# Optimization experiments

Measured on AMD Instinct MI355X. Metric: run time of the kernel, lower is better.

## Reference

```python
import jax, jax.numpy as jnp
import numpy as np

D_MODEL = 1024
N_HEADS = 16
D_K = D_MODEL // N_HEADS


def setup_inputs() -> dict:
    key = jax.random.key(0)
    ks = jax.random.split(key, 12)
    B, S, D = 4, 2048, D_MODEL
    scale = 1.0 / np.sqrt(D)
    inp = {
        'query': jax.random.normal(ks[0], (B, S, D), jnp.float32),
        'key': jax.random.normal(ks[1], (B, S, D), jnp.float32),
        'value': jax.random.normal(ks[2], (B, S, D), jnp.float32),
        'Wq': jax.random.normal(ks[3], (D, D), jnp.float32) * scale,
        'bq': jax.random.normal(ks[4], (D,), jnp.float32) * 0.02,
        'Wk': jax.random.normal(ks[5], (D, D), jnp.float32) * scale,
        'bk': jax.random.normal(ks[6], (D,), jnp.float32) * 0.02,
        'Wv': jax.random.normal(ks[7], (D, D), jnp.float32) * scale,
        'bv': jax.random.normal(ks[8], (D,), jnp.float32) * 0.02,
        'Wo': jax.random.normal(ks[9], (D, D), jnp.float32) * scale,
        'bo': jax.random.normal(ks[10], (D,), jnp.float32) * 0.02,
    }
    return inp


def reference(query, key, value, Wq, bq, Wk, bk, Wv, bv, Wo, bo):
    B, S, D = query.shape
    # torch nn.Linear: y = x @ W^T + b
    def proj(x, W, b):
        y = jnp.einsum('bsd,ed->bse', x, W) + b
        # [B,S,D] -> [B,H,S,d_k]
        return y.reshape(B, S, N_HEADS, D_K).transpose(0, 2, 1, 3)

    q = proj(query, Wq, bq)
    k = proj(key, Wk, bk)
    v = proj(value, Wv, bv)

    scores = jnp.einsum('bhqd,bhkd->bhqk', q, k) / jnp.sqrt(jnp.float32(D_K))
    attn = jax.nn.softmax(scores, axis=-1)  # dropout = identity (eval mode)
    out = jnp.einsum('bhqk,bhkd->bhqd', attn, v)
    out = out.transpose(0, 2, 1, 3).reshape(B, S, D)
    return jnp.einsum('bsd,ed->bse', out, Wo) + bo
```

## Files before the change

### kernel.cpp

```cpp
#include <hip/hip_runtime.h>
#include <hip/hip_bf16.h>
#include <cstdint>
#include <cstddef>


#define BATCH   4
#define SEQ     2048
#define D_MODEL 1024
#define NHEADS  16
#define DK      64

typedef __attribute__((ext_vector_type(8))) __bf16 bf16x8_t;
typedef __attribute__((ext_vector_type(4))) float  f32x4;

__device__ inline unsigned int pack2(float lo, float hi) {
  __hip_bfloat162 h = __float22bfloat162_rn(make_float2(lo, hi));
  union { __hip_bfloat162 h; unsigned int u; } c; c.h = h; return c.u;
}
__device__ inline unsigned short f2bf(float f) { return (unsigned short)pack2(f, f); }

#if __has_builtin(__builtin_amdgcn_exp2f)
__device__ inline float fexp2(float x) { return __builtin_amdgcn_exp2f(x); }
#else
__device__ inline float fexp2(float x) { return __expf(x * 0.6931471805599453f); }
#endif

__device__ inline void cvt8(const float* __restrict__ s, unsigned short* __restrict__ d) {
  const float4 a = *(const float4*)s;
  const float4 b = *(const float4*)(s + 4);
  uint4 r;
  r.x = pack2(a.x, a.y); r.y = pack2(a.z, a.w);
  r.z = pack2(b.x, b.y); r.w = pack2(b.z, b.w);
  *(uint4*)d = r;
}

typedef __attribute__((address_space(3))) unsigned int lds_u32_t;
typedef const __attribute__((address_space(1))) unsigned int glb_u32_t;
__device__ inline void gld16(const unsigned short* g, unsigned short* l) {
  __builtin_amdgcn_global_load_lds((glb_u32_t*)(uintptr_t)g,
                                   (lds_u32_t*)(unsigned int)(uintptr_t)l, 16, 0, 0);
}

__global__ __launch_bounds__(256) void cvt3_kernel(
    const float* __restrict__ a, const float* __restrict__ b, const float* __restrict__ c,
    unsigned short* __restrict__ oa, unsigned short* __restrict__ ob, unsigned short* __restrict__ oc)
{
  const float* s = (blockIdx.y == 0) ? a : (blockIdx.y == 1) ? b : c;
  unsigned short* d = (blockIdx.y == 0) ? oa : (blockIdx.y == 1) ? ob : oc;
  const size_t i = ((size_t)blockIdx.x * 256 + threadIdx.x) * 8;
  cvt8(s + i, d + i);
}
__global__ __launch_bounds__(256) void cvt4_kernel(
    const float* __restrict__ a, const float* __restrict__ b,
    const float* __restrict__ c, const float* __restrict__ dd,
    unsigned short* __restrict__ oa, unsigned short* __restrict__ ob,
    unsigned short* __restrict__ oc, unsigned short* __restrict__ od)
{
  const float* s = (blockIdx.y == 0) ? a : (blockIdx.y == 1) ? b : (blockIdx.y == 2) ? c : dd;
  unsigned short* d = (blockIdx.y == 0) ? oa : (blockIdx.y == 1) ? ob : (blockIdx.y == 2) ? oc : od;
  const size_t i = ((size_t)blockIdx.x * 256 + threadIdx.x) * 8;
  cvt8(s + i, d + i);
}

__device__ inline void gemm_core(const unsigned short* __restrict__ A,
                                 const unsigned short* __restrict__ W,
                                 unsigned short* a_lds, unsigned short* b_lds,
                                 int m0, int n0, f32x4 (&acc)[4][4])
{
  const int tid  = threadIdx.x;
  const int lane = tid & 63;
  const int wv   = tid >> 6;
  const int l15  = lane & 15;
  const int quad = lane >> 4;
  const int wm = (wv & 1) * 64;
  const int wn = (wv >> 1) * 64;

  const int srow = tid >> 2;
  const int sch  = (tid & 3) ^ (srow & 3);
  const unsigned short* Ap0 = A + (size_t)(m0 + srow) * D_MODEL + sch * 8;
  const unsigned short* Ap1 = Ap0 + (size_t)64 * D_MODEL;
  const unsigned short* Wp0 = W + (size_t)(n0 + srow) * D_MODEL + sch * 8;
  const unsigned short* Wp1 = Wp0 + (size_t)64 * D_MODEL;
  unsigned short* al0 = a_lds + wv * 512;
  unsigned short* al1 = a_lds + 2048 + wv * 512;
  unsigned short* bl0 = b_lds + wv * 512;
  unsigned short* bl1 = b_lds + 2048 + wv * 512;

  const int pq = (quad ^ (l15 & 3)) * 8;

  for (int k0 = 0; k0 < D_MODEL; k0 += 32) {
    __syncthreads();
    gld16(Ap0 + k0, al0);
    gld16(Ap1 + k0, al1);
    gld16(Wp0 + k0, bl0);
    gld16(Wp1 + k0, bl1);
    __syncthreads();

    bf16x8_t af[4], bfr[4];
#pragma unroll
    for (int i = 0; i < 4; ++i)
      af[i] = *(const bf16x8_t*)&a_lds[(wm + i * 16 + l15) * 32 + pq];
#pragma unroll
    for (int j = 0; j < 4; ++j)
      bfr[j] = *(const bf16x8_t*)&b_lds[(wn + j * 16 + l15) * 32 + pq];

#pragma unroll
    for (int i = 0; i < 4; ++i)
#pragma unroll
      for (int j = 0; j < 4; ++j)
        acc[i][j] = __builtin_amdgcn_mfma_f32_16x16x32_bf16(af[i], bfr[j], acc[i][j], 0, 0, 0);
  }
}

__global__ __launch_bounds__(256) void qkv_kernel(
    const unsigned short* __restrict__ qb, const unsigned short* __restrict__ kb,
    const unsigned short* __restrict__ vb,
    const unsigned short* __restrict__ wq, const unsigned short* __restrict__ wk,
    const unsigned short* __restrict__ wvp,
    const float* __restrict__ bq, const float* __restrict__ bk, const float* __restrict__ bv,
    unsigned short* __restrict__ Qws, unsigned short* __restrict__ Kws,
    unsigned short* __restrict__ Vws)
{
  __shared__ unsigned short a_lds[128 * 32];
  __shared__ unsigned short b_lds[128 * 32];

  const int z = blockIdx.z;
  const unsigned short* A = (z == 0) ? qb : (z == 1) ? kb : vb;
  const unsigned short* W = (z == 0) ? wq : (z == 1) ? wk : wvp;
  const float* bias       = (z == 0) ? bq : (z == 1) ? bk : bv;
  unsigned short* C       = (z == 0) ? Qws : (z == 1) ? Kws : Vws;
  const int m0 = blockIdx.x * 128;
  const int n0 = blockIdx.y * 128;

  f32x4 acc[4][4];
#pragma unroll
  for (int i = 0; i < 4; ++i)
#pragma unroll
    for (int j = 0; j < 4; ++j)
      acc[i][j] = (f32x4){0.f, 0.f, 0.f, 0.f};

  gemm_core(A, W, a_lds, b_lds, m0, n0, acc);

  const int tid  = threadIdx.x;
  const int lane = tid & 63;
  const int wv   = tid >> 6;
  const int l15  = lane & 15;
  const int quad = lane >> 4;
  const int wm = (wv & 1) * 64;
  const int wn = (wv >> 1) * 64;
  if (z == 2) {
    for (int j = 0; j < 4; ++j) {
      const int n = n0 + wn + j * 16 + l15;
      const int hh = n >> 6, dd = n & 63;
      const float bvl = bias[n];
      for (int i = 0; i < 4; ++i) {
        const int mbase = m0 + wm + i * 16 + quad * 4;
        const int bb = mbase >> 11, ss = mbase & 2047;
        uint2 w2 = make_uint2(pack2(acc[i][j][0] + bvl, acc[i][j][1] + bvl),
                              pack2(acc[i][j][2] + bvl, acc[i][j][3] + bvl));
        *(uint2*)(C + (((size_t)bb * NHEADS + hh) * DK + dd) * SEQ + ss) = w2;
      }
    }
  } else {
    const float oscale = (z == 0) ? 0.18033688011112042f : 1.0f;
    for (int j = 0; j < 4; ++j) {
      const int n = n0 + wn + j * 16 + l15;
      const int hh = n >> 6, dd = n & 63;
      const float bvl = bias[n];
      for (int i = 0; i < 4; ++i) {
        const int mbase = m0 + wm + i * 16 + quad * 4;
        const int bb = mbase >> 11, ss = mbase & 2047;
        unsigned short* dst = C + (((size_t)bb * NHEADS + hh) * SEQ + ss) * DK + dd;
        for (int r = 0; r < 4; ++r)
          dst[(size_t)r * DK] = f2bf((acc[i][j][r] + bvl) * oscale);
      }
    }
  }
}

__global__ __launch_bounds__(256) void outproj_kernel(
    const unsigned short* __restrict__ A, const unsigned short* __restrict__ W,
    const float* __restrict__ bias, float* __restrict__ C)
{
  __shared__ unsigned short a_lds[128 * 32];
  __shared__ unsigned short b_lds[128 * 32];
  const int m0 = blockIdx.x * 128;
  const int n0 = blockIdx.y * 128;

  f32x4 acc[4][4];
#pragma unroll
  for (int i = 0; i < 4; ++i)
#pragma unroll
    for (int j = 0; j < 4; ++j)
      acc[i][j] = (f32x4){0.f, 0.f, 0.f, 0.f};

  gemm_core(A, W, a_lds, b_lds, m0, n0, acc);

  const int tid  = threadIdx.x;
  const int lane = tid & 63;
  const int wv   = tid >> 6;
  const int l15  = lane & 15;
  const int quad = lane >> 4;
  const int wm = (wv & 1) * 64;
  const int wn = (wv >> 1) * 64;
  for (int j = 0; j < 4; ++j) {
    const int n = n0 + wn + j * 16 + l15;
    const float bvl = bias[n];
    for (int i = 0; i < 4; ++i) {
      const int mbase = m0 + wm + i * 16 + quad * 4;
      for (int r = 0; r < 4; ++r)
        C[(size_t)(mbase + r) * D_MODEL + n] = acc[i][j][r] + bvl;
    }
  }
}

__global__ __launch_bounds__(256) void attn_kernel(
    const unsigned short* __restrict__ Q,
    const unsigned short* __restrict__ K,
    const unsigned short* __restrict__ Vt,
    unsigned short* __restrict__ Oattn)
{
  __shared__ unsigned short k_sw[64 * 64];
  __shared__ unsigned short vt_sw[64 * 64];
  __shared__ unsigned short pt_sw[4 * 16 * 64];

  const int tid  = threadIdx.x;
  const int lane = tid & 63;
  const int wv   = tid >> 6;
  const int l15  = lane & 15;
  const int quad = lane >> 4;
  const int bh   = blockIdx.x;
  const int q0   = blockIdx.y * 64;
  const size_t hoff = (size_t)bh * SEQ * DK;
  const unsigned short* Qh  = Q  + hoff;
  const unsigned short* Kh  = K  + hoff;
  const unsigned short* Vth = Vt + hoff;

  bf16x8_t qf0, qf1;
  {
    const unsigned short* qr = Qh + (size_t)(q0 + wv * 16 + l15) * DK;
    qf0 = *(const bf16x8_t*)(qr + quad * 8);
    qf1 = *(const bf16x8_t*)(qr + 32 + quad * 8);
  }

  f32x4 o[4];
#pragma unroll
  for (int t = 0; t < 4; ++t) o[t] = (f32x4){0.f, 0.f, 0.f, 0.f};
  float mval = -1e30f, lval = 0.f;

  const int sr = lane >> 3;
  const int pc = lane & 7;
  const int r0 = wv * 16 + sr;
  const int r1 = r0 + 8;
  const int sem0 = pc ^ (r0 & 7) ^ (r0 >> 3);
  const int sem1 = pc ^ (r1 & 7) ^ (r1 >> 3);
  const unsigned short* Ks0 = Kh  + (size_t)r0 * DK  + sem0 * 8;
  const unsigned short* Ks1 = Kh  + (size_t)r1 * DK  + sem1 * 8;
  const unsigned short* Vs0 = Vth + (size_t)r0 * SEQ + sem0 * 8;
  const unsigned short* Vs1 = Vth + (size_t)r1 * SEQ + sem1 * 8;
  unsigned short* kd0 = k_sw  + wv * 1024;
  unsigned short* kd1 = k_sw  + wv * 1024 + 512;
  unsigned short* vd0 = vt_sw + wv * 1024;
  unsigned short* vd1 = vt_sw + wv * 1024 + 512;

  const int swz_l15 = (l15 & 7) ^ (l15 >> 3);
  unsigned short* pt_base = pt_sw + wv * 1024;

  for (int kb = 0; kb < SEQ / 64; ++kb) {
    const int key0 = kb * 64;
    __syncthreads();
    gld16(Ks0 + (size_t)key0 * DK, kd0);
    gld16(Ks1 + (size_t)key0 * DK, kd1);
    gld16(Vs0 + key0, vd0);
    gld16(Vs1 + key0, vd1);
    __syncthreads();

    f32x4 s[4];
#pragma unroll
    for (int t = 0; t < 4; ++t) {
      const int row = t * 16 + l15;
      const int sw  = (row & 7) ^ (row >> 3);
      bf16x8_t kf0 = *(const bf16x8_t*)&k_sw[row * 64 + ((quad ^ sw) << 3)];
      bf16x8_t kf1 = *(const bf16x8_t*)&k_sw[row * 64 + (((quad | 4) ^ sw) << 3)];
      f32x4 z = (f32x4){0.f, 0.f, 0.f, 0.f};
      z = __builtin_amdgcn_mfma_f32_16x16x32_bf16(kf0, qf0, z, 0, 0, 0);
      z = __builtin_amdgcn_mfma_f32_16x16x32_bf16(kf1, qf1, z, 0, 0, 0);
      s[t] = z;
    }

    float mx = s[0][0];
#pragma unroll
    for (int t = 0; t < 4; ++t)
#pragma unroll
      for (int r = 0; r < 4; ++r) mx = fmaxf(mx, s[t][r]);
    mx = fmaxf(mx, __shfl_xor(mx, 16));
    mx = fmaxf(mx, __shfl_xor(mx, 32));
    const float mnew  = fmaxf(mval, mx);
    const float alpha = fexp2(mval - mnew);
    mval = mnew;
    float rs = 0.f;
    float p[4][4];
#pragma unroll
    for (int t = 0; t < 4; ++t)
#pragma unroll
      for (int r = 0; r < 4; ++r) { p[t][r] = fexp2(s[t][r] - mnew); rs += p[t][r]; }
    rs += __shfl_xor(rs, 16);
    rs += __shfl_xor(rs, 32);
    lval = lval * alpha + rs;
#pragma unroll
    for (int t = 0; t < 4; ++t) o[t] *= alpha;

#pragma unroll
    for (int t = 0; t < 4; ++t) {
      const int chunk = 2 * t + (quad >> 1);
      unsigned short* dst = pt_base + l15 * 64 + ((chunk ^ swz_l15) << 3) + (quad & 1) * 4;
      *(uint2*)dst = make_uint2(pack2(p[t][0], p[t][1]), pack2(p[t][2], p[t][3]));
    }
    asm volatile("s_waitcnt lgkmcnt(0)" ::: "memory");

    bf16x8_t pf0 = *(const bf16x8_t*)(pt_base + l15 * 64 + ((quad ^ swz_l15) << 3));
    bf16x8_t pf1 = *(const bf16x8_t*)(pt_base + l15 * 64 + (((quad | 4) ^ swz_l15) << 3));

#pragma unroll
    for (int nt = 0; nt < 4; ++nt) {
      const int row = nt * 16 + l15;
      const int sw  = (row & 7) ^ (row >> 3);
      bf16x8_t vf0 = *(const bf16x8_t*)&vt_sw[row * 64 + ((quad ^ sw) << 3)];
      bf16x8_t vf1 = *(const bf16x8_t*)&vt_sw[row * 64 + (((quad | 4) ^ sw) << 3)];
      o[nt] = __builtin_amdgcn_mfma_f32_16x16x32_bf16(vf0, pf0, o[nt], 0, 0, 0);
      o[nt] = __builtin_amdgcn_mfma_f32_16x16x32_bf16(vf1, pf1, o[nt], 0, 0, 0);
    }
  }

  const int bb = bh >> 4, hh = bh & 15;
  const float inv = 1.0f / lval;
  unsigned short* orow = Oattn + (size_t)(bb * SEQ + q0 + wv * 16 + l15) * D_MODEL + hh * DK + quad * 4;
#pragma unroll
  for (int nt = 0; nt < 4; ++nt) {
    f32x4 v = o[nt];
    *(uint2*)(orow + nt * 16) = make_uint2(pack2(v[0] * inv, v[1] * inv),
                                           pack2(v[2] * inv, v[3] * inv));
  }
}

extern "C" void kernel_launch(void* const* d_in, const int* in_sizes, int n_in,
                              void* d_out, int out_size, void* d_ws, size_t ws_size,
                              hipStream_t stream) {
  const float* query = (const float*)d_in[0];
  const float* key   = (const float*)d_in[1];
  const float* value = (const float*)d_in[2];
  const float* Wq    = (const float*)d_in[3];
  const float* bq    = (const float*)d_in[4];
  const float* Wk    = (const float*)d_in[5];
  const float* bk    = (const float*)d_in[6];
  const float* Wv    = (const float*)d_in[7];
  const float* bv    = (const float*)d_in[8];
  const float* Wo    = (const float*)d_in[9];
  const float* bo    = (const float*)d_in[10];

  const size_t E  = (size_t)BATCH * SEQ * D_MODEL;
  const size_t WE = (size_t)D_MODEL * D_MODEL;
  unsigned short* ws  = (unsigned short*)d_ws;
  unsigned short* Qws = ws;
  unsigned short* Kws = ws + E;
  unsigned short* Vws = ws + 2 * E;
  unsigned short* qb  = ws + 3 * E;
  unsigned short* kb  = ws + 4 * E;
  unsigned short* vb  = ws + 5 * E;
  unsigned short* wqb = ws + 6 * E;
  unsigned short* wkb = wqb + WE;
  unsigned short* wvb = wqb + 2 * WE;
  unsigned short* wob = wqb + 3 * WE;
  unsigned short* Aws = qb;

  cvt3_kernel<<<dim3(E / 2048, 3), 256, 0, stream>>>(query, key, value, qb, kb, vb);
  cvt4_kernel<<<dim3(WE / 2048, 4), 256, 0, stream>>>(Wq, Wk, Wv, Wo, wqb, wkb, wvb, wob);

  qkv_kernel<<<dim3(BATCH * SEQ / 128, D_MODEL / 128, 3), 256, 0, stream>>>(
      qb, kb, vb, wqb, wkb, wvb, bq, bk, bv, Qws, Kws, Vws);
  attn_kernel<<<dim3(BATCH * NHEADS, SEQ / 64), 256, 0, stream>>>(Qws, Kws, Vws, Aws);
  outproj_kernel<<<dim3(BATCH * SEQ / 128, D_MODEL / 128), 256, 0, stream>>>(
      Aws, wob, bo, (float*)d_out);
}
```

Before: 410.2 us.

## Double-buffer K/V tiles, lazily rescale softmax, and raise MFMA wave priority

The attention kernel now keeps two LDS buffers for K and V^T. It issues the global-to-LDS loads for the next key block before computing on the current one, which drops from two barriers per iteration to one. The online-softmax rescale of the output accumulator and running sum now runs only when some lane's block max exceeds the running max by more than 8 (log2 domain). Otherwise the stale max is kept and the exp/multiply work per block is skipped. s_setprio brackets the MFMA sections to favour matrix issue. The cost is double the K/V LDS footprint, which may lower occupancy, and unnormalised P values up to 2^8 before bf16 packing.

```diff
diff --git a/kernel.cpp b/kernel.cpp
--- a/kernel.cpp
+++ b/kernel.cpp
@@ -220,8 +220,8 @@
     const unsigned short* __restrict__ Vt,
     unsigned short* __restrict__ Oattn)
 {
-  __shared__ unsigned short k_sw[64 * 64];
-  __shared__ unsigned short vt_sw[64 * 64];
+  __shared__ unsigned short k_sw[2 * 64 * 64];
+  __shared__ unsigned short vt_sw[2 * 64 * 64];
   __shared__ unsigned short pt_sw[4 * 16 * 64];
 
   const int tid  = threadIdx.x;
@@ -254,39 +254,47 @@
   const int r1 = r0 + 8;
   const int sem0 = pc ^ (r0 & 7) ^ (r0 >> 3);
   const int sem1 = pc ^ (r1 & 7) ^ (r1 >> 3);
-  const unsigned short* Ks0 = Kh  + (size_t)r0 * DK  + sem0 * 8;
-  const unsigned short* Ks1 = Kh  + (size_t)r1 * DK  + sem1 * 8;
-  const unsigned short* Vs0 = Vth + (size_t)r0 * SEQ + sem0 * 8;
-  const unsigned short* Vs1 = Vth + (size_t)r1 * SEQ + sem1 * 8;
-  unsigned short* kd0 = k_sw  + wv * 1024;
-  unsigned short* kd1 = k_sw  + wv * 1024 + 512;
-  unsigned short* vd0 = vt_sw + wv * 1024;
-  unsigned short* vd1 = vt_sw + wv * 1024 + 512;
+  const unsigned short* KsA = Kh  + (size_t)r0 * DK  + sem0 * 8;
+  const unsigned short* KsB = Kh  + (size_t)r1 * DK  + sem1 * 8;
+  const unsigned short* VsA = Vth + (size_t)r0 * SEQ + sem0 * 8;
+  const unsigned short* VsB = Vth + (size_t)r1 * SEQ + sem1 * 8;
+  unsigned short* kd = k_sw  + wv * 1024;
+  unsigned short* vd = vt_sw + wv * 1024;
+
+#define STAGE(buf, key0) do {                                        \
+    gld16(KsA + (size_t)(key0) * DK, kd + (buf) * 4096);             \
+    gld16(KsB + (size_t)(key0) * DK, kd + (buf) * 4096 + 512);       \
+    gld16(VsA + (key0),              vd + (buf) * 4096);             \
+    gld16(VsB + (key0),              vd + (buf) * 4096 + 512);       \
+  } while (0)
 
   const int swz_l15 = (l15 & 7) ^ (l15 >> 3);
   unsigned short* pt_base = pt_sw + wv * 1024;
 
+  STAGE(0, 0);
+  __syncthreads();
+
+  int cur = 0;
   for (int kb = 0; kb < SEQ / 64; ++kb) {
-    const int key0 = kb * 64;
-    __syncthreads();
-    gld16(Ks0 + (size_t)key0 * DK, kd0);
-    gld16(Ks1 + (size_t)key0 * DK, kd1);
-    gld16(Vs0 + key0, vd0);
-    gld16(Vs1 + key0, vd1);
-    __syncthreads();
+    if (kb + 1 < SEQ / 64) STAGE(cur ^ 1, (kb + 1) * 64);
+
+    const unsigned short* kcur = k_sw  + cur * 4096;
+    const unsigned short* vcur = vt_sw + cur * 4096;
 
     f32x4 s[4];
+    __builtin_amdgcn_s_setprio(1);
 #pragma unroll
     for (int t = 0; t < 4; ++t) {
       const int row = t * 16 + l15;
       const int sw  = (row & 7) ^ (row >> 3);
-      bf16x8_t kf0 = *(const bf16x8_t*)&k_sw[row * 64 + ((quad ^ sw) << 3)];
-      bf16x8_t kf1 = *(const bf16x8_t*)&k_sw[row * 64 + (((quad | 4) ^ sw) << 3)];
+      bf16x8_t kf0 = *(const bf16x8_t*)&kcur[row * 64 + ((quad ^ sw) << 3)];
+      bf16x8_t kf1 = *(const bf16x8_t*)&kcur[row * 64 + (((quad | 4) ^ sw) << 3)];
       f32x4 z = (f32x4){0.f, 0.f, 0.f, 0.f};
       z = __builtin_amdgcn_mfma_f32_16x16x32_bf16(kf0, qf0, z, 0, 0, 0);
       z = __builtin_amdgcn_mfma_f32_16x16x32_bf16(kf1, qf1, z, 0, 0, 0);
       s[t] = z;
     }
+    __builtin_amdgcn_s_setprio(0);
 
     float mx = s[0][0];
 #pragma unroll
@@ -295,20 +303,23 @@
       for (int r = 0; r < 4; ++r) mx = fmaxf(mx, s[t][r]);
     mx = fmaxf(mx, __shfl_xor(mx, 16));
     mx = fmaxf(mx, __shfl_xor(mx, 32));
-    const float mnew  = fmaxf(mval, mx);
-    const float alpha = fexp2(mval - mnew);
-    mval = mnew;
+    if (__any(mx > mval + 8.0f)) {
+      const float mnew  = fmaxf(mval, mx);
+      const float alpha = fexp2(mval - mnew);
+      mval = mnew;
+      lval *= alpha;
+#pragma unroll
+      for (int t = 0; t < 4; ++t) o[t] *= alpha;
+    }
     float rs = 0.f;
     float p[4][4];
 #pragma unroll
     for (int t = 0; t < 4; ++t)
 #pragma unroll
-      for (int r = 0; r < 4; ++r) { p[t][r] = fexp2(s[t][r] - mnew); rs += p[t][r]; }
+      for (int r = 0; r < 4; ++r) { p[t][r] = fexp2(s[t][r] - mval); rs += p[t][r]; }
     rs += __shfl_xor(rs, 16);
     rs += __shfl_xor(rs, 32);
-    lval = lval * alpha + rs;
-#pragma unroll
-    for (int t = 0; t < 4; ++t) o[t] *= alpha;
+    lval += rs;
 
 #pragma unroll
     for (int t = 0; t < 4; ++t) {
@@ -321,16 +332,22 @@
     bf16x8_t pf0 = *(const bf16x8_t*)(pt_base + l15 * 64 + ((quad ^ swz_l15) << 3));
     bf16x8_t pf1 = *(const bf16x8_t*)(pt_base + l15 * 64 + (((quad | 4) ^ swz_l15) << 3));
 
+    __builtin_amdgcn_s_setprio(1);
 #pragma unroll
     for (int nt = 0; nt < 4; ++nt) {
       const int row = nt * 16 + l15;
       const int sw  = (row & 7) ^ (row >> 3);
-      bf16x8_t vf0 = *(const bf16x8_t*)&vt_sw[row * 64 + ((quad ^ sw) << 3)];
-      bf16x8_t vf1 = *(const bf16x8_t*)&vt_sw[row * 64 + (((quad | 4) ^ sw) << 3)];
+      bf16x8_t vf0 = *(const bf16x8_t*)&vcur[row * 64 + ((quad ^ sw) << 3)];
+      bf16x8_t vf1 = *(const bf16x8_t*)&vcur[row * 64 + (((quad | 4) ^ sw) << 3)];
       o[nt] = __builtin_amdgcn_mfma_f32_16x16x32_bf16(vf0, pf0, o[nt], 0, 0, 0);
       o[nt] = __builtin_amdgcn_mfma_f32_16x16x32_bf16(vf1, pf1, o[nt], 0, 0, 0);
     }
-  }
+    __builtin_amdgcn_s_setprio(0);
+
+    __syncthreads();
+    cur ^= 1;
+  }
+#undef STAGE
 
   const int bb = bh >> 4, hh = bh & 15;
   const float inv = 1.0f / lval;
```

After: 399.5 us. 1.03x faster.
